# Optimization experiments

Measured on AMD Instinct MI355X. Metric: run time of the kernel, lower is better.

Reference implementation:

```python
import jax, jax.numpy as jnp
import numpy as np

N_USERS = 6144
N_ITEMS = 12288
N_NODES = N_USERS + N_ITEMS
D = 64
AVG_DEG = 32
NNZ = N_NODES * AVG_DEG
N_LAYERS = 2
K = 30  # module keeps top (k+1) per row


def setup_inputs() -> dict:
    key = jax.random.key(0)
    k1, k2, k3, k4, k5 = jax.random.split(key, 5)
    user_emb = 0.1 * jax.random.normal(k1, (N_USERS, D), dtype=jnp.float32)
    item_emb = 0.1 * jax.random.normal(k2, (N_ITEMS, D), dtype=jnp.float32)
    edge_row = jax.random.randint(k3, (NNZ,), 0, N_NODES, dtype=jnp.int32)
    edge_col = jax.random.randint(k4, (NNZ,), 0, N_NODES, dtype=jnp.int32)
    # normalized-adjacency-like values (positive, ~1/deg scale)
    edge_val = jax.random.uniform(k5, (NNZ,), dtype=jnp.float32) / AVG_DEG
    return {
        "user_emb": user_emb,
        "item_emb": item_emb,
        "edge_row": edge_row,
        "edge_col": edge_col,
        "edge_val": edge_val,
    }


def _spmm(edge_row, edge_col, edge_val, x):
    # y[r] = sum_{(r,c) in E} val * x[c]   -- torch.sparse.mm equivalent (COO)
    return jax.ops.segment_sum(edge_val[:, None] * x[edge_col], edge_row,
                               num_segments=N_NODES)


def reference(user_emb, item_emb, edge_row, edge_col, edge_val):
    # LightGCN propagation
    all_emb = jnp.concatenate([user_emb, item_emb], axis=0)  # [N, D]
    embs = [all_emb]
    for _ in range(N_LAYERS):
        all_emb = _spmm(edge_row, edge_col, edge_val, all_emb)
        embs.append(all_emb)
    light_out = jnp.mean(jnp.stack(embs, axis=1), axis=1)  # [N, D]

    items = light_out[N_USERS:]  # [N_ITEMS, D]
    # F.normalize(dim=1, p=2) with eps clamp
    norm = jnp.linalg.norm(items, axis=1, keepdims=True)
    items = items / jnp.maximum(norm, 1e-12)

    # dense pairwise similarity
    sim = items @ items.T  # [N_ITEMS, N_ITEMS]

    # top_k: keep top (k+1) values per row, zero elsewhere
    vals, idx = jax.lax.top_k(sim, K + 1)  # [N_ITEMS, K+1]
    rows = jnp.arange(sim.shape[0])[:, None]
    sparse_sim = jnp.zeros_like(sim).at[rows, idx].set(vals)

    # apply_non_linearity('relu', i) -> relu
    return jax.nn.relu(sparse_sim)
```

## Files before the change

### kernel.cpp

```cpp
#include <hip/hip_runtime.h>
#include <hip/hip_bf16.h>

#define N_USERS 6144
#define N_ITEMS 12288
#define N_NODES 18432
#define D 64
#define NNZ 589824
#define K_TOP 31
#define NCAND_MIN 48
#define NCAND_MAX 240
#define CMAX 256

using frag_ab = __attribute__((ext_vector_type(8))) short;
using frag_cd = __attribute__((ext_vector_type(4))) float;

__device__ inline ushort f32_to_bf16_bits(float f) {
    unsigned b = __float_as_uint(f);
    unsigned r = (b + 0x7FFFu + ((b >> 16) & 1u)) >> 16;
    return (ushort)r;
}

__global__ void concat64_kernel(const float* __restrict__ u,
                                const float* __restrict__ it,
                                double* __restrict__ e0) {
    int i = blockIdx.x * 256 + threadIdx.x;
    const int NU = N_USERS * D;
    e0[i] = (i < NU) ? (double)u[i] : (double)it[i - NU];
}

__global__ void count_kernel(const int* __restrict__ er, int* __restrict__ cnt) {
    int e = blockIdx.x * 256 + threadIdx.x;
    atomicAdd(&cnt[er[e]], 1);
}

__global__ __launch_bounds__(256) void scan_kernel(const int* __restrict__ cnt,
                                                   int* __restrict__ row_start,
                                                   int* __restrict__ cursor) {
    __shared__ int part[256];
    int t = threadIdx.x;
    const int PER = N_NODES / 256;
    int s = 0;
    for (int i = 0; i < PER; ++i) s += cnt[t * PER + i];
    part[t] = s;
    __syncthreads();
    for (int off = 1; off < 256; off <<= 1) {
        int v = part[t];
        int w = (t >= off) ? part[t - off] : 0;
        __syncthreads();
        part[t] = v + w;
        __syncthreads();
    }
    int run = (t == 0) ? 0 : part[t - 1];
    for (int i = 0; i < PER; ++i) {
        int idx = t * PER + i;
        row_start[idx] = run;
        cursor[idx] = run;
        run += cnt[idx];
    }
    if (t == 255) row_start[N_NODES] = run;
}

__global__ void scatter_kernel(const int* __restrict__ er, const int* __restrict__ ec,
                               const float* __restrict__ ev,
                               int* __restrict__ cursor,
                               int* __restrict__ ecol_s, float* __restrict__ eval_s) {
    int e = blockIdx.x * 256 + threadIdx.x;
    int r = er[e];
    int pos = atomicAdd(&cursor[r], 1);
    ecol_s[pos] = ec[e];
    eval_s[pos] = ev[e];
}

__global__ __launch_bounds__(256) void spmm_csr_kernel(const int* __restrict__ row_start,
                                                       const int* __restrict__ ecol_s,
                                                       const float* __restrict__ eval_s,
                                                       const double* __restrict__ x,
                                                       double* __restrict__ y) {
    int t = threadIdx.x;
    int lane = t & 63, wave = t >> 6;
    int row = blockIdx.x * 4 + wave;
    if (row >= N_NODES) return;
    int beg = row_start[row], end = row_start[row + 1];
    double acc = 0.0;
    for (int j = beg; j < end; ++j) {
        int c = ecol_s[j];
        double v = (double)eval_s[j];
        acc += v * x[(size_t)c * D + lane];
    }
    y[(size_t)row * D + lane] = acc;
}

__global__ void mean_norm64_kernel(const double* __restrict__ e0,
                                   const double* __restrict__ e1,
                                   const double* __restrict__ e2,
                                   double* __restrict__ xn64,
                                   ushort* __restrict__ xh) {
    int t = threadIdx.x;
    int wave = t >> 6, lane = t & 63;
    int r = blockIdx.x * 4 + wave;
    size_t g = (size_t)(r + N_USERS) * D + lane;
    double s = (e0[g] + e1[g] + e2[g]) / 3.0;
    double ss = s * s;
    #pragma unroll
    for (int off = 32; off; off >>= 1) ss += __shfl_xor(ss, off);
    double norm = sqrt(ss);
    double denom = fmax(norm, 1e-12);
    double v = s / denom;
    xn64[(size_t)r * D + lane] = v;
    xh[(size_t)r * D + lane] = f32_to_bf16_bits((float)v);
}

#define LDS_STRIDE 72
__global__ __launch_bounds__(256) void simgemm_kernel(const ushort* __restrict__ Xh,
                                                      ushort* __restrict__ Cb) {
    __shared__ __align__(16) ushort Als[128 * LDS_STRIDE];
    __shared__ __align__(16) ushort Bls[128 * LDS_STRIDE];
    int t = threadIdx.x;
    int bi = blockIdx.y, bj = blockIdx.x;

    #pragma unroll
    for (int p = 0; p < 4; ++p) {
        int u4 = t + 256 * p;
        int row = u4 >> 3;
        int seg = u4 & 7;
        *(uint4*)&Als[row * LDS_STRIDE + seg * 8] =
            *(const uint4*)&Xh[(size_t)(bi * 128 + row) * D + seg * 8];
        *(uint4*)&Bls[row * LDS_STRIDE + seg * 8] =
            *(const uint4*)&Xh[(size_t)(bj * 128 + row) * D + seg * 8];
    }
    __syncthreads();

    int lane = t & 63, wave = t >> 6;
    int wrow = (wave >> 1) * 64, wcol = (wave & 1) * 64;
    int ml = lane & 15, quad = lane >> 4;

    frag_cd acc[4][4] = {};
    #pragma unroll
    for (int s = 0; s < 2; ++s) {
        frag_ab af[4], bf[4];
        int koff = s * 32 + quad * 8;
        #pragma unroll
        for (int rt = 0; rt < 4; ++rt)
            af[rt] = *(const frag_ab*)&Als[(wrow + rt * 16 + ml) * LDS_STRIDE + koff];
        #pragma unroll
        for (int ct = 0; ct < 4; ++ct)
            bf[ct] = *(const frag_ab*)&Bls[(wcol + ct * 16 + ml) * LDS_STRIDE + koff];
        #pragma unroll
        for (int rt = 0; rt < 4; ++rt)
            #pragma unroll
            for (int ct = 0; ct < 4; ++ct)
                acc[rt][ct] = __builtin_amdgcn_mfma_f32_16x16x32_bf16(
                    af[rt], bf[ct], acc[rt][ct], 0, 0, 0);
    }

    #pragma unroll
    for (int rt = 0; rt < 4; ++rt) {
        #pragma unroll
        for (int ct = 0; ct < 4; ++ct) {
            size_t gr = (size_t)(bi * 128 + wrow + rt * 16 + quad * 4);
            int    gc = bj * 128 + wcol + ct * 16 + ml;
            #pragma unroll
            for (int r = 0; r < 4; ++r)
                Cb[(gr + r) * N_ITEMS + gc] = f32_to_bf16_bits(acc[rt][ct][r]);
        }
    }
}

__global__ __launch_bounds__(256) void topk_kernel(const ushort* __restrict__ Cb,
                                                   float* __restrict__ Cout,
                                                   const double* __restrict__ xn64) {
    __shared__ int s_red[4];
    __shared__ unsigned s_cnt;
    __shared__ int    candi[CMAX];
    __shared__ double candv[CMAX];
    __shared__ double s_xr[D];
    int t = threadIdx.x;
    int r = blockIdx.x;
    const uint4* Crow4 = (const uint4*)(Cb + (size_t)r * N_ITEMS);

    unsigned short u[48];
    #pragma unroll
    for (int j = 0; j < 6; ++j) {
        uint4 f = Crow4[t + 256 * j];
        const unsigned* w = &f.x;
        #pragma unroll
        for (int q = 0; q < 4; ++q) {
            unsigned lo = w[q] & 0xFFFFu, hi = w[q] >> 16;
            u[j * 8 + 2 * q]     = (unsigned short)(lo ^ ((lo & 0x8000u) ? 0xFFFFu : 0x8000u));
            u[j * 8 + 2 * q + 1] = (unsigned short)(hi ^ ((hi & 0x8000u) ? 0xFFFFu : 0x8000u));
        }
    }
    if (t < D) s_xr[t] = xn64[(size_t)r * D + t];

    unsigned lo = 0u, hi = 0xFFFFu, T = 0u, bestT = 0u;
    int found = 0;
    for (int it = 0; it < 16; ++it) {
        if (found || lo > hi) { __syncthreads(); __syncthreads(); continue; }
        unsigned mid = lo + ((hi - lo) >> 1);
        int c = 0;
        #pragma unroll
        for (int k = 0; k < 48; ++k) c += (u[k] >= mid) ? 1 : 0;
        #pragma unroll
        for (int off = 32; off; off >>= 1) c += __shfl_down(c, off);
        if ((t & 63) == 0) s_red[t >> 6] = c;
        __syncthreads();
        int ctot = s_red[0] + s_red[1] + s_red[2] + s_red[3];
        __syncthreads();
        if (ctot >= NCAND_MIN) {
            bestT = mid;
            if (ctot <= NCAND_MAX) { T = mid; found = 1; }
            else lo = mid + 1;
        } else {
            if (mid == 0u) { lo = 1u; hi = 0u; }
            else hi = mid - 1;
        }
    }
    if (!found) T = bestT;

    if (t == 0) s_cnt = 0;
    __syncthreads();
    #pragma unroll
    for (int k = 0; k < 48; ++k) {
        if (u[k] >= (unsigned short)T) {
            unsigned pos = atomicAdd(&s_cnt, 1u);
            if (pos < CMAX) candi[pos] = 8 * (t + 256 * (k >> 3)) + (k & 7);
        }
    }
    __syncthreads();
    int c = (int)s_cnt; if (c > CMAX) c = CMAX;

    if (t < c) {
        const double* xc = xn64 + (size_t)candi[t] * D;
        double acc = 0.0;
        #pragma unroll 8
        for (int k = 0; k < D; ++k) acc += s_xr[k] * xc[k];
        candv[t] = acc;
    }
    __syncthreads();

    int   sel_idx = -1;
    float sel_val = 0.f;
    if (t < c) {
        double v = candv[t];
        int    id = candi[t];
        int rank = 0;
        for (int j = 0; j < c; ++j) {
            double vj = candv[j];
            rank += (vj > v || (vj == v && candi[j] < id)) ? 1 : 0;
        }
        if (rank < K_TOP) {
            sel_idx = id;
            sel_val = (v > 0.0) ? (float)v : 0.f;
        }
    }

    float4* Orow4 = (float4*)(Cout + (size_t)r * N_ITEMS);
    float4 z = make_float4(0.f, 0.f, 0.f, 0.f);
    #pragma unroll
    for (int j = 0; j < 12; ++j) Orow4[t + 256 * j] = z;
    __syncthreads();
    if (sel_idx >= 0) Cout[(size_t)r * N_ITEMS + sel_idx] = sel_val;
}

extern "C" void kernel_launch(void* const* d_in, const int* in_sizes, int n_in,
                              void* d_out, int out_size, void* d_ws, size_t ws_size,
                              hipStream_t stream) {
    const float* user_emb = (const float*)d_in[0];
    const float* item_emb = (const float*)d_in[1];
    const int*   edge_row = (const int*)d_in[2];
    const int*   edge_col = (const int*)d_in[3];
    const float* edge_val = (const float*)d_in[4];
    float* C = (float*)d_out;

    double* e0d  = (double*)d_ws;
    double* e1d  = e0d + (size_t)N_NODES * D;
    double* e2d  = e1d + (size_t)N_NODES * D;
    double* xn64 = e2d + (size_t)N_NODES * D;
    ushort* xh   = (ushort*)(xn64 + (size_t)N_ITEMS * D);
    ushort* Cb   = xh + (size_t)N_ITEMS * D;
    float*  eval_s = (float*)(Cb + (size_t)N_ITEMS * N_ITEMS);
    int*    ecol_s = (int*)(eval_s + NNZ);
    int*    cnt       = ecol_s + NNZ;
    int*    row_start = cnt + N_NODES;
    int*    cursor    = row_start + N_NODES + 1;

    hipMemsetAsync(cnt, 0, N_NODES * sizeof(int), stream);

    concat64_kernel<<<N_NODES * D / 256, 256, 0, stream>>>(user_emb, item_emb, e0d);

    count_kernel<<<NNZ / 256, 256, 0, stream>>>(edge_row, cnt);
    scan_kernel<<<1, 256, 0, stream>>>(cnt, row_start, cursor);
    scatter_kernel<<<NNZ / 256, 256, 0, stream>>>(edge_row, edge_col, edge_val,
                                                  cursor, ecol_s, eval_s);

    spmm_csr_kernel<<<(N_NODES + 3) / 4, 256, 0, stream>>>(row_start, ecol_s, eval_s, e0d, e1d);
    spmm_csr_kernel<<<(N_NODES + 3) / 4, 256, 0, stream>>>(row_start, ecol_s, eval_s, e1d, e2d);

    mean_norm64_kernel<<<N_ITEMS / 4, 256, 0, stream>>>(e0d, e1d, e2d, xn64, xh);

    dim3 ggrid(N_ITEMS / 128, N_ITEMS / 128);
    simgemm_kernel<<<ggrid, 256, 0, stream>>>(xh, Cb);

    topk_kernel<<<N_ITEMS, 256, 0, stream>>>(Cb, C, xn64);
}
```

Before: 1.004 ms.

## Fuse similarity GEMM with per-segment candidate selection, drop dense bf16 matrix

Replaces the separate similarity GEMM, which wrote a full bf16 N_ITEMS x N_ITEMS matrix, and the top-k kernel, which reread it. A fused kernel now computes 128-row tiles across 8 column segments and keeps per-row candidates in LDS, pruning them with a threshold bisection when a row overflows. A finalize kernel merges the per-segment candidates, recomputes exact fp64 dot products and ranks the top 31. The SpMM also packs column and value into int2 and unrolls with four accumulators. This removes about 300MB of intermediate traffic but adds serialized LDS-atomic selection loops with barriers and lowers the grid to 768 blocks.

```diff
diff --git a/kernel.cpp b/kernel.cpp
--- a/kernel.cpp
+++ b/kernel.cpp
@@ -7,17 +7,22 @@
 #define D 64
 #define NNZ 589824
 #define K_TOP 31
-#define NCAND_MIN 48
-#define NCAND_MAX 240
-#define CMAX 256
+#define SEG 8
+#define SEG_COLS (N_ITEMS / SEG)
+#define CAP 64
+#define KEEP 48
+#define SELCAP 128
 
 using frag_ab = __attribute__((ext_vector_type(8))) short;
 using frag_cd = __attribute__((ext_vector_type(4))) float;
 
-__device__ inline ushort f32_to_bf16_bits(float f) {
+__device__ inline unsigned f32_to_bf16_bits(float f) {
     unsigned b = __float_as_uint(f);
-    unsigned r = (b + 0x7FFFu + ((b >> 16) & 1u)) >> 16;
-    return (ushort)r;
+    return (b + 0x7FFFu + ((b >> 16) & 1u)) >> 16;
+}
+__device__ inline unsigned bf16_key(float f) {
+    unsigned k = f32_to_bf16_bits(f) & 0xFFFFu;
+    return k ^ ((k & 0x8000u) ? 0xFFFFu : 0x8000u);
 }
 
 __global__ void concat64_kernel(const float* __restrict__ u,
@@ -62,18 +67,15 @@
 
 __global__ void scatter_kernel(const int* __restrict__ er, const int* __restrict__ ec,
                                const float* __restrict__ ev,
-                               int* __restrict__ cursor,
-                               int* __restrict__ ecol_s, float* __restrict__ eval_s) {
+                               int* __restrict__ cursor, int2* __restrict__ ep) {
     int e = blockIdx.x * 256 + threadIdx.x;
     int r = er[e];
     int pos = atomicAdd(&cursor[r], 1);
-    ecol_s[pos] = ec[e];
-    eval_s[pos] = ev[e];
+    ep[pos] = make_int2(ec[e], __float_as_int(ev[e]));
 }
 
 __global__ __launch_bounds__(256) void spmm_csr_kernel(const int* __restrict__ row_start,
-                                                       const int* __restrict__ ecol_s,
-                                                       const float* __restrict__ eval_s,
+                                                       const int2* __restrict__ ep,
                                                        const double* __restrict__ x,
                                                        double* __restrict__ y) {
     int t = threadIdx.x;
@@ -81,13 +83,21 @@
     int row = blockIdx.x * 4 + wave;
     if (row >= N_NODES) return;
     int beg = row_start[row], end = row_start[row + 1];
-    double acc = 0.0;
-    for (int j = beg; j < end; ++j) {
-        int c = ecol_s[j];
-        double v = (double)eval_s[j];
-        acc += v * x[(size_t)c * D + lane];
-    }
-    y[(size_t)row * D + lane] = acc;
+    double a0 = 0.0, a1 = 0.0, a2 = 0.0, a3 = 0.0;
+    int j = beg;
+    int n4 = beg + ((end - beg) & ~3);
+    for (; j < n4; j += 4) {
+        int2 p0 = ep[j], p1 = ep[j + 1], p2 = ep[j + 2], p3 = ep[j + 3];
+        a0 += (double)__int_as_float(p0.y) * x[(size_t)p0.x * D + lane];
+        a1 += (double)__int_as_float(p1.y) * x[(size_t)p1.x * D + lane];
+        a2 += (double)__int_as_float(p2.y) * x[(size_t)p2.x * D + lane];
+        a3 += (double)__int_as_float(p3.y) * x[(size_t)p3.x * D + lane];
+    }
+    for (; j < end; ++j) {
+        int2 p = ep[j];
+        a0 += (double)__int_as_float(p.y) * x[(size_t)p.x * D + lane];
+    }
+    y[(size_t)row * D + lane] = (a0 + a1) + (a2 + a3);
 }
 
 __global__ void mean_norm64_kernel(const double* __restrict__ e0,
@@ -107,159 +117,202 @@
     double denom = fmax(norm, 1e-12);
     double v = s / denom;
     xn64[(size_t)r * D + lane] = v;
-    xh[(size_t)r * D + lane] = f32_to_bf16_bits((float)v);
-}
-
-#define LDS_STRIDE 72
-__global__ __launch_bounds__(256) void simgemm_kernel(const ushort* __restrict__ Xh,
-                                                      ushort* __restrict__ Cb) {
-    __shared__ __align__(16) ushort Als[128 * LDS_STRIDE];
-    __shared__ __align__(16) ushort Bls[128 * LDS_STRIDE];
-    int t = threadIdx.x;
-    int bi = blockIdx.y, bj = blockIdx.x;
-
+    xh[(size_t)r * D + lane] = (ushort)f32_to_bf16_bits((float)v);
+}
+
+__global__ __launch_bounds__(256) void gemm_select_kernel(const ushort* __restrict__ Xh,
+                                                          unsigned* __restrict__ candbuf,
+                                                          int* __restrict__ candcnt) {
+    __shared__ unsigned s_buf[128 * CAP];
+    __shared__ int      s_cnt[128];
+    __shared__ unsigned s_thr[128];
+    __shared__ int      s_of;
+    int t = threadIdx.x;
+    int seg = blockIdx.x, rb = blockIdx.y;
+    int lane = t & 63, wave = t >> 6;
+    int wrowG = (wave >> 1) * 64, wcolG = (wave & 1) * 64;
+    int ml = lane & 15, quad = lane >> 4;
+
+    if (t < 128) { s_cnt[t] = 0; s_thr[t] = 0; }
+
+    frag_ab afr[4][2];
     #pragma unroll
-    for (int p = 0; p < 4; ++p) {
-        int u4 = t + 256 * p;
-        int row = u4 >> 3;
-        int seg = u4 & 7;
-        *(uint4*)&Als[row * LDS_STRIDE + seg * 8] =
-            *(const uint4*)&Xh[(size_t)(bi * 128 + row) * D + seg * 8];
-        *(uint4*)&Bls[row * LDS_STRIDE + seg * 8] =
-            *(const uint4*)&Xh[(size_t)(bj * 128 + row) * D + seg * 8];
-    }
-    __syncthreads();
-
-    int lane = t & 63, wave = t >> 6;
-    int wrow = (wave >> 1) * 64, wcol = (wave & 1) * 64;
-    int ml = lane & 15, quad = lane >> 4;
-
-    frag_cd acc[4][4] = {};
-    #pragma unroll
-    for (int s = 0; s < 2; ++s) {
-        frag_ab af[4], bf[4];
-        int koff = s * 32 + quad * 8;
-        #pragma unroll
-        for (int rt = 0; rt < 4; ++rt)
-            af[rt] = *(const frag_ab*)&Als[(wrow + rt * 16 + ml) * LDS_STRIDE + koff];
+    for (int rt = 0; rt < 4; ++rt)
+        #pragma unroll
+        for (int s = 0; s < 2; ++s)
+            afr[rt][s] = *(const frag_ab*)&Xh[(size_t)(rb * 128 + wrowG + rt * 16 + ml) * D
+                                              + s * 32 + quad * 8];
+    __syncthreads();
+
+    for (int tt = 0; tt < SEG_COLS / 128; ++tt) {
+        int tilebase = seg * SEG_COLS + tt * 128;
+        frag_ab bfr[4][2];
         #pragma unroll
         for (int ct = 0; ct < 4; ++ct)
-            bf[ct] = *(const frag_ab*)&Bls[(wcol + ct * 16 + ml) * LDS_STRIDE + koff];
-        #pragma unroll
-        for (int rt = 0; rt < 4; ++rt)
             #pragma unroll
-            for (int ct = 0; ct < 4; ++ct)
-                acc[rt][ct] = __builtin_amdgcn_mfma_f32_16x16x32_bf16(
-                    af[rt], bf[ct], acc[rt][ct], 0, 0, 0);
-    }
-
-    #pragma unroll
-    for (int rt = 0; rt < 4; ++rt) {
-        #pragma unroll
-        for (int ct = 0; ct < 4; ++ct) {
-            size_t gr = (size_t)(bi * 128 + wrow + rt * 16 + quad * 4);
-            int    gc = bj * 128 + wcol + ct * 16 + ml;
+            for (int s = 0; s < 2; ++s)
+                bfr[ct][s] = *(const frag_ab*)&Xh[(size_t)(tilebase + wcolG + ct * 16 + ml) * D
+                                                  + s * 32 + quad * 8];
+        frag_cd acc[4][4] = {};
+        #pragma unroll
+        for (int s = 0; s < 2; ++s)
             #pragma unroll
-            for (int r = 0; r < 4; ++r)
-                Cb[(gr + r) * N_ITEMS + gc] = f32_to_bf16_bits(acc[rt][ct][r]);
+            for (int rt = 0; rt < 4; ++rt)
+                #pragma unroll
+                for (int ct = 0; ct < 4; ++ct)
+                    acc[rt][ct] = __builtin_amdgcn_mfma_f32_16x16x32_bf16(
+                        afr[rt][s], bfr[ct][s], acc[rt][ct], 0, 0, 0);
+
+        unsigned long long pend = ~0ull;
+        for (int it = 0; it < 8; ++it) {
+            if (t == 0) s_of = 0;
+            __syncthreads();
+            #pragma unroll
+            for (int rt = 0; rt < 4; ++rt) {
+                #pragma unroll
+                for (int ct = 0; ct < 4; ++ct) {
+                    #pragma unroll
+                    for (int rg = 0; rg < 4; ++rg) {
+                        int b = rt * 16 + ct * 4 + rg;
+                        if ((pend >> b) & 1ull) {
+                            float v = acc[rt][ct][rg];
+                            unsigned key = bf16_key(v);
+                            int row = wrowG + rt * 16 + quad * 4 + rg;
+                            if (key >= s_thr[row]) {
+                                int pos = atomicAdd(&s_cnt[row], 1);
+                                if (pos < CAP) {
+                                    s_buf[row * CAP + pos] =
+                                        (key << 16) | (unsigned)(tilebase + wcolG + ct * 16 + ml);
+                                    pend &= ~(1ull << b);
+                                }
+                            } else pend &= ~(1ull << b);
+                        }
+                    }
+                }
+            }
+            __syncthreads();
+            if (t < 128 && s_cnt[t] > CAP) {
+                int rr = t;
+                int n = CAP;
+                unsigned lo = 0, hi = 0xFFFFu;
+                while (lo < hi) {
+                    unsigned mid = (lo + hi + 1) >> 1;
+                    int cc = 0;
+                    for (int i = 0; i < n; ++i) cc += ((s_buf[rr * CAP + i] >> 16) >= mid);
+                    if (cc >= KEEP) lo = mid; else hi = mid - 1;
+                }
+                unsigned T = lo;
+                int k = 0;
+                for (int i = 0; i < n; ++i) {
+                    unsigned e = s_buf[rr * CAP + i];
+                    if ((e >> 16) >= T) s_buf[rr * CAP + (k++)] = e;
+                }
+                s_cnt[rr] = k; s_thr[rr] = T;
+                s_of = 1;
+            }
+            __syncthreads();
+            if (!s_of) break;
         }
     }
-}
-
-__global__ __launch_bounds__(256) void topk_kernel(const ushort* __restrict__ Cb,
-                                                   float* __restrict__ Cout,
-                                                   const double* __restrict__ xn64) {
+
+    if (t < 128) {
+        int row = t;
+        int c = s_cnt[row]; if (c > CAP) c = CAP;
+        int g = rb * 128 + row;
+        candcnt[g * SEG + seg] = c;
+        for (int i = 0; i < c; ++i)
+            candbuf[(size_t)g * (SEG * CAP) + seg * CAP + i] = s_buf[row * CAP + i];
+    }
+}
+
+__global__ __launch_bounds__(256) void finalize_kernel(const unsigned* __restrict__ candbuf,
+                                                       const int* __restrict__ candcnt,
+                                                       const double* __restrict__ xn64,
+                                                       float* __restrict__ out) {
+    __shared__ unsigned L[SEG * CAP];
+    __shared__ int s_base[SEG + 1];
     __shared__ int s_red[4];
-    __shared__ unsigned s_cnt;
-    __shared__ int    candi[CMAX];
-    __shared__ double candv[CMAX];
-    __shared__ double s_xr[D];
+    __shared__ unsigned s_selent[SELCAP];
+    __shared__ double   s_selv[SELCAP];
+    __shared__ double   s_xr[D];
+    __shared__ int s_selcnt;
     int t = threadIdx.x;
     int r = blockIdx.x;
-    const uint4* Crow4 = (const uint4*)(Cb + (size_t)r * N_ITEMS);
-
-    unsigned short u[48];
-    #pragma unroll
-    for (int j = 0; j < 6; ++j) {
-        uint4 f = Crow4[t + 256 * j];
-        const unsigned* w = &f.x;
-        #pragma unroll
-        for (int q = 0; q < 4; ++q) {
-            unsigned lo = w[q] & 0xFFFFu, hi = w[q] >> 16;
-            u[j * 8 + 2 * q]     = (unsigned short)(lo ^ ((lo & 0x8000u) ? 0xFFFFu : 0x8000u));
-            u[j * 8 + 2 * q + 1] = (unsigned short)(hi ^ ((hi & 0x8000u) ? 0xFFFFu : 0x8000u));
-        }
+
+    if (t == 0) {
+        int acc = 0;
+        #pragma unroll
+        for (int s = 0; s < SEG; ++s) { s_base[s] = acc; acc += candcnt[r * SEG + s]; }
+        s_base[SEG] = acc;
     }
     if (t < D) s_xr[t] = xn64[(size_t)r * D + t];
-
-    unsigned lo = 0u, hi = 0xFFFFu, T = 0u, bestT = 0u;
-    int found = 0;
+    __syncthreads();
+    int M = s_base[SEG];
+
+    for (int ti = t; ti < SEG * CAP; ti += 256) {
+        int seg = ti >> 6, i = ti & (CAP - 1);
+        int c = s_base[seg + 1] - s_base[seg];
+        if (i < c) L[s_base[seg] + i] = candbuf[(size_t)r * (SEG * CAP) + seg * CAP + i];
+    }
+    __syncthreads();
+
+    unsigned lo = 0, hi = 0xFFFFu;
     for (int it = 0; it < 16; ++it) {
-        if (found || lo > hi) { __syncthreads(); __syncthreads(); continue; }
-        unsigned mid = lo + ((hi - lo) >> 1);
-        int c = 0;
-        #pragma unroll
-        for (int k = 0; k < 48; ++k) c += (u[k] >= mid) ? 1 : 0;
-        #pragma unroll
-        for (int off = 32; off; off >>= 1) c += __shfl_down(c, off);
-        if ((t & 63) == 0) s_red[t >> 6] = c;
+        if (lo >= hi) { __syncthreads(); __syncthreads(); continue; }
+        unsigned mid = (lo + hi + 1) >> 1;
+        int cc = 0;
+        for (int i = t; i < M; i += 256) cc += ((L[i] >> 16) >= mid);
+        #pragma unroll
+        for (int off = 32; off; off >>= 1) cc += __shfl_down(cc, off);
+        if ((t & 63) == 0) s_red[t >> 6] = cc;
         __syncthreads();
         int ctot = s_red[0] + s_red[1] + s_red[2] + s_red[3];
         __syncthreads();
-        if (ctot >= NCAND_MIN) {
-            bestT = mid;
-            if (ctot <= NCAND_MAX) { T = mid; found = 1; }
-            else lo = mid + 1;
-        } else {
-            if (mid == 0u) { lo = 1u; hi = 0u; }
-            else hi = mid - 1;
+        if (ctot >= KEEP) lo = mid; else hi = mid - 1;
+    }
+    unsigned T = lo;
+
+    if (t == 0) s_selcnt = 0;
+    __syncthreads();
+    for (int i = t; i < M; i += 256) {
+        unsigned e = L[i];
+        if ((e >> 16) >= T) {
+            int p = atomicAdd(&s_selcnt, 1);
+            if (p < SELCAP) s_selent[p] = e;
         }
     }
-    if (!found) T = bestT;
-
-    if (t == 0) s_cnt = 0;
-    __syncthreads();
+    __syncthreads();
+    int c = s_selcnt; if (c > SELCAP) c = SELCAP;
+
+    if (t < c) {
+        int col = s_selent[t] & 0xFFFFu;
+        const double* xc = xn64 + (size_t)col * D;
+        double a = 0.0;
+        #pragma unroll 8
+        for (int k = 0; k < D; ++k) a += s_xr[k] * xc[k];
+        s_selv[t] = a;
+    }
+    __syncthreads();
+
+    float4* O4 = (float4*)(out + (size_t)r * N_ITEMS);
+    float4 z = make_float4(0.f, 0.f, 0.f, 0.f);
     #pragma unroll
-    for (int k = 0; k < 48; ++k) {
-        if (u[k] >= (unsigned short)T) {
-            unsigned pos = atomicAdd(&s_cnt, 1u);
-            if (pos < CMAX) candi[pos] = 8 * (t + 256 * (k >> 3)) + (k & 7);
-        }
-    }
-    __syncthreads();
-    int c = (int)s_cnt; if (c > CMAX) c = CMAX;
-
+    for (int j = 0; j < 12; ++j) O4[t + 256 * j] = z;
+
+    int sel_col = -1; float sel_val = 0.f;
     if (t < c) {
-        const double* xc = xn64 + (size_t)candi[t] * D;
-        double acc = 0.0;
-        #pragma unroll 8
-        for (int k = 0; k < D; ++k) acc += s_xr[k] * xc[k];
-        candv[t] = acc;
-    }
-    __syncthreads();
-
-    int   sel_idx = -1;
-    float sel_val = 0.f;
-    if (t < c) {
-        double v = candv[t];
-        int    id = candi[t];
+        double v = s_selv[t];
+        int myc = (int)(s_selent[t] & 0xFFFFu);
         int rank = 0;
         for (int j = 0; j < c; ++j) {
-            double vj = candv[j];
-            rank += (vj > v || (vj == v && candi[j] < id)) ? 1 : 0;
+            double vj = s_selv[j];
+            int cj = (int)(s_selent[j] & 0xFFFFu);
+            rank += (vj > v || (vj == v && cj < myc)) ? 1 : 0;
         }
-        if (rank < K_TOP) {
-            sel_idx = id;
-            sel_val = (v > 0.0) ? (float)v : 0.f;
-        }
-    }
-
-    float4* Orow4 = (float4*)(Cout + (size_t)r * N_ITEMS);
-    float4 z = make_float4(0.f, 0.f, 0.f, 0.f);
-    #pragma unroll
-    for (int j = 0; j < 12; ++j) Orow4[t + 256 * j] = z;
-    __syncthreads();
-    if (sel_idx >= 0) Cout[(size_t)r * N_ITEMS + sel_idx] = sel_val;
+        if (rank < K_TOP) { sel_col = myc; sel_val = (v > 0.0) ? (float)v : 0.f; }
+    }
+    __syncthreads();
+    if (sel_col >= 0) out[(size_t)r * N_ITEMS + sel_col] = sel_val;
 }
 
 extern "C" void kernel_launch(void* const* d_in, const int* in_sizes, int n_in,
@@ -276,13 +329,13 @@
     double* e1d  = e0d + (size_t)N_NODES * D;
     double* e2d  = e1d + (size_t)N_NODES * D;
     double* xn64 = e2d + (size_t)N_NODES * D;
-    ushort* xh   = (ushort*)(xn64 + (size_t)N_ITEMS * D);
-    ushort* Cb   = xh + (size_t)N_ITEMS * D;
-    float*  eval_s = (float*)(Cb + (size_t)N_ITEMS * N_ITEMS);
-    int*    ecol_s = (int*)(eval_s + NNZ);
-    int*    cnt       = ecol_s + NNZ;
-    int*    row_start = cnt + N_NODES;
-    int*    cursor    = row_start + N_NODES + 1;
+    int2*   ep   = (int2*)(xn64 + (size_t)N_ITEMS * D);
+    ushort* xh   = (ushort*)(ep + NNZ);
+    unsigned* candbuf = (unsigned*)(xh + (size_t)N_ITEMS * D);
+    int*  candcnt   = (int*)(candbuf + (size_t)N_ITEMS * SEG * CAP);
+    int*  cnt       = candcnt + (size_t)N_ITEMS * SEG;
+    int*  row_start = cnt + N_NODES;
+    int*  cursor    = row_start + N_NODES + 1;
 
     hipMemsetAsync(cnt, 0, N_NODES * sizeof(int), stream);
 
@@ -290,16 +343,15 @@
 
     count_kernel<<<NNZ / 256, 256, 0, stream>>>(edge_row, cnt);
     scan_kernel<<<1, 256, 0, stream>>>(cnt, row_start, cursor);
-    scatter_kernel<<<NNZ / 256, 256, 0, stream>>>(edge_row, edge_col, edge_val,
-                                                  cursor, ecol_s, eval_s);
-
-    spmm_csr_kernel<<<(N_NODES + 3) / 4, 256, 0, stream>>>(row_start, ecol_s, eval_s, e0d, e1d);
-    spmm_csr_kernel<<<(N_NODES + 3) / 4, 256, 0, stream>>>(row_start, ecol_s, eval_s, e1d, e2d);
+    scatter_kernel<<<NNZ / 256, 256, 0, stream>>>(edge_row, edge_col, edge_val, cursor, ep);
+
+    spmm_csr_kernel<<<(N_NODES + 3) / 4, 256, 0, stream>>>(row_start, ep, e0d, e1d);
+    spmm_csr_kernel<<<(N_NODES + 3) / 4, 256, 0, stream>>>(row_start, ep, e1d, e2d);
 
     mean_norm64_kernel<<<N_ITEMS / 4, 256, 0, stream>>>(e0d, e1d, e2d, xn64, xh);
 
-    dim3 ggrid(N_ITEMS / 128, N_ITEMS / 128);
-    simgemm_kernel<<<ggrid, 256, 0, stream>>>(xh, Cb);
-
-    topk_kernel<<<N_ITEMS, 256, 0, stream>>>(Cb, C, xn64);
-}
+    dim3 ggrid(SEG, N_ITEMS / 128);
+    gemm_select_kernel<<<ggrid, 256, 0, stream>>>(xh, candbuf, candcnt);
+
+    finalize_kernel<<<N_ITEMS, 256, 0, stream>>>(candbuf, candcnt, xn64, C);
+}
```

Measured after the change: 2.138 ms. 113% more time.
